# Optimization experiments

Measured on AMD Instinct MI355X. Metric: run time of the kernel, lower is better.

## Reference

```python
import jax, jax.numpy as jnp
import numpy as np

N_NODES = 100000
N_EDGES = 1000000
IN_DIM, HID_DIM, OUT_DIM = 64, 64, 128


def gcn_conv(x, W, b, src, dst, deg_inv_sqrt, n_nodes):
    # PyG GCNConv: x' = D^{-1/2} (A + I) D^{-1/2} (x W) + b
    xw = x @ W  # [N, out]
    norm = deg_inv_sqrt[src] * deg_inv_sqrt[dst]  # [E'] (edges incl. self-loops)
    msgs = xw[src] * norm[:, None]  # gather + scale, [E', out]
    out = jax.ops.segment_sum(msgs, dst, num_segments=n_nodes)
    return out + b


def setup_inputs() -> dict:
    key = jax.random.key(0)
    ks = jax.random.split(key, 8)
    x = jax.random.normal(ks[0], (N_NODES, IN_DIM), dtype=jnp.float32)
    edge_index = jax.random.randint(ks[1], (2, N_EDGES), 0, N_NODES, dtype=jnp.int64 if jax.config.read('jax_enable_x64') else jnp.int32)
    # Glorot-ish init for weights, zeros for biases (matches GCNConv defaults)
    def glorot(k, fan_in, fan_out):
        s = jnp.sqrt(6.0 / (fan_in + fan_out))
        return jax.random.uniform(k, (fan_in, fan_out), jnp.float32, -s, s)
    return {
        "x": x,
        "W1": glorot(ks[2], IN_DIM, HID_DIM), "b1": jnp.zeros((HID_DIM,), jnp.float32),
        "W2": glorot(ks[3], HID_DIM, HID_DIM), "b2": jnp.zeros((HID_DIM,), jnp.float32),
        "W3": glorot(ks[4], HID_DIM, OUT_DIM), "b3": jnp.zeros((OUT_DIM,), jnp.float32),
        "edge_index": edge_index,
    }


def reference(x, W1, b1, W2, b2, W3, b3, edge_index):
    n = x.shape[0]
    loop = jnp.arange(n, dtype=edge_index.dtype)
    src = jnp.concatenate([edge_index[0], loop])  # add self-loops
    dst = jnp.concatenate([edge_index[1], loop])
    deg = jax.ops.segment_sum(jnp.ones_like(dst, dtype=x.dtype), dst, num_segments=n)
    deg_inv_sqrt = jnp.where(deg > 0, jax.lax.rsqrt(deg), 0.0)
    # Dropout(p=0.5) is identity in eval mode
    h = jax.nn.relu(gcn_conv(x, W1, b1, src, dst, deg_inv_sqrt, n))
    h = jax.nn.relu(gcn_conv(h, W2, b2, src, dst, deg_inv_sqrt, n))
    return gcn_conv(h, W3, b3, src, dst, deg_inv_sqrt, n)
```

## Files before the change

### kernel.cpp

```cpp
#include <hip/hip_runtime.h>
#include <hip/hip_fp16.h>


#define NBMAX 512
#define EPB   4096


__global__ __launch_bounds__(256) void bin_hist(const int* __restrict__ dst,
                                                int* __restrict__ hist, int E, int NB) {
  __shared__ int cnt[NBMAX];
  for (int i = threadIdx.x; i < NB; i += 256) cnt[i] = 0;
  __syncthreads();
  int base = blockIdx.x * EPB;
  for (int it = 0; it < EPB; it += 256) {
    int e = base + it + threadIdx.x;
    if (e < E) atomicAdd(&cnt[dst[e] >> 8], 1);
  }
  __syncthreads();
  for (int i = threadIdx.x; i < NB; i += 256) hist[(size_t)blockIdx.x * NB + i] = cnt[i];
}

__global__ __launch_bounds__(256) void bucket_prefix(int* __restrict__ hist,
                                                     int* __restrict__ bucket_tot,
                                                     int nblk, int NB) {
  __shared__ int tmp[256];
  int b = blockIdx.x;
  int t = threadIdx.x;
  int v = (t < nblk) ? hist[(size_t)t * NB + b] : 0;
  tmp[t] = v;
  __syncthreads();
  for (int off = 1; off < 256; off <<= 1) {
    int a = (t >= off) ? tmp[t - off] : 0;
    __syncthreads();
    tmp[t] += a;
    __syncthreads();
  }
  if (t < nblk) hist[(size_t)t * NB + b] = tmp[t] - v;
  if (t == 255) bucket_tot[b] = tmp[255];
}

__global__ __launch_bounds__(512) void bucket_scan(const int* __restrict__ bucket_tot,
                                                   int* __restrict__ bucket_off, int NB, int E) {
  __shared__ int tmp[NBMAX];
  int t = threadIdx.x;
  int v = (t < NB) ? bucket_tot[t] : 0;
  tmp[t] = v;
  __syncthreads();
  for (int off = 1; off < 512; off <<= 1) {
    int a = (t >= off) ? tmp[t - off] : 0;
    __syncthreads();
    tmp[t] += a;
    __syncthreads();
  }
  if (t < NB) bucket_off[t] = tmp[t] - v;
  if (t == 0) bucket_off[NB] = E;
}

__global__ __launch_bounds__(256) void bin_scatter(const int* __restrict__ src,
                                                   const int* __restrict__ dst,
                                                   const int* __restrict__ chunk_excl,
                                                   const int* __restrict__ bucket_off,
                                                   int2* __restrict__ pairs, int E, int NB) {
  __shared__ int cur[NBMAX];
  for (int i = threadIdx.x; i < NB; i += 256)
    cur[i] = bucket_off[i] + chunk_excl[(size_t)blockIdx.x * NB + i];
  __syncthreads();
  int base = blockIdx.x * EPB;
  for (int it = 0; it < EPB; it += 256) {
    int e = base + it + threadIdx.x;
    if (e < E) {
      int d = dst[e];
      int pos = atomicAdd(&cur[d >> 8], 1);
      pairs[pos] = make_int2(src[e], d);
    }
  }
}

__global__ __launch_bounds__(256) void bucket_fill(const int2* __restrict__ pairs,
                                                   const int* __restrict__ bucket_off,
                                                   int* __restrict__ row_ptr,
                                                   int* __restrict__ csr_src,
                                                   float* __restrict__ dis, int n, int NB) {
  __shared__ int cnt[256];
  __shared__ int tmp[256];
  __shared__ int cur[256];
  int b = blockIdx.x;
  int t = threadIdx.x;
  int node_base = b << 8;
  int ebeg = bucket_off[b];
  int eend = bucket_off[b + 1];
  cnt[t] = 0;
  __syncthreads();
  for (int e = ebeg + t; e < eend; e += 256) {
    atomicAdd(&cnt[pairs[e].y - node_base], 1);
  }
  __syncthreads();
  int v = cnt[t];
  tmp[t] = v;
  __syncthreads();
  for (int off = 1; off < 256; off <<= 1) {
    int a = (t >= off) ? tmp[t - off] : 0;
    __syncthreads();
    tmp[t] += a;
    __syncthreads();
  }
  int excl = tmp[t] - v;
  int node = node_base + t;
  if (node < n) {
    row_ptr[node] = ebeg + excl;
    dis[node] = rsqrtf((float)v + 1.0f);
  }
  cur[t] = ebeg + excl;
  if (b == NB - 1 && t == 0) row_ptr[n] = eend;
  __syncthreads();
  for (int e = ebeg + t; e < eend; e += 256) {
    int2 p = pairs[e];
    int pos = atomicAdd(&cur[p.y - node_base], 1);
    csr_src[pos] = p.x;
  }
}


__device__ __forceinline__ unsigned int packh(float a, float b) {
  unsigned int lo = (unsigned int)__half_as_ushort(__float2half_rn(a));
  unsigned int hi = (unsigned int)__half_as_ushort(__float2half_rn(b));
  return lo | (hi << 16);
}

__device__ __forceinline__ void unpack_add(float& x0, float& x1, unsigned int u) {
  x0 += __half2float(__ushort_as_half((unsigned short)(u & 0xffffu)));
  x1 += __half2float(__ushort_as_half((unsigned short)(u >> 16)));
}


__global__ void prescale_h(const float* __restrict__ x, const float* __restrict__ dis,
                           unsigned short* __restrict__ xs, int n) {
  int i = blockIdx.x * blockDim.x + threadIdx.x;
  if (i >= n * 8) return;
  int row = i >> 3;
  float s = dis[row];
  const float4* p = (const float4*)(x + (size_t)i * 8);
  float4 f0 = p[0];
  float4 f1 = p[1];
  uint4 u;
  u.x = packh(f0.x * s, f0.y * s);
  u.y = packh(f0.z * s, f0.w * s);
  u.z = packh(f1.x * s, f1.y * s);
  u.w = packh(f1.z * s, f1.w * s);
  *(uint4*)(xs + (size_t)i * 8) = u;
}


__global__ __launch_bounds__(256) void gather64q(const int* __restrict__ row_ptr,
                                                 const int* __restrict__ csr_src,
                                                 const unsigned short* __restrict__ in,
                                                 const float* __restrict__ dis,
                                                 float* __restrict__ agg, int n) {
  int node = blockIdx.x * 16 + (threadIdx.x >> 4);
  int l15 = threadIdx.x & 15;
  int gbase = threadIdx.x & 48;
  if (node >= n) return;

  int beg = row_ptr[node];
  int end = row_ptr[node + 1];

  float a0 = 0.f, a1 = 0.f, a2 = 0.f, a3 = 0.f;

  {
    uint2 q = *(const uint2*)(in + (size_t)node * 64 + l15 * 4);
    unpack_add(a0, a1, q.x); unpack_add(a2, a3, q.y);
  }

  for (int kb = beg; kb < end; kb += 16) {
    int idx = (kb + l15 < end) ? csr_src[kb + l15] : 0;
    int cnt = end - kb; if (cnt > 16) cnt = 16;
    int rr = 0;
    for (; rr + 2 <= cnt; rr += 2) {
      int s0 = __shfl(idx, gbase + rr);
      int s1 = __shfl(idx, gbase + rr + 1);
      uint2 q0 = *(const uint2*)(in + (size_t)s0 * 64 + l15 * 4);
      uint2 q1 = *(const uint2*)(in + (size_t)s1 * 64 + l15 * 4);
      unpack_add(a0, a1, q0.x); unpack_add(a2, a3, q0.y);
      unpack_add(a0, a1, q1.x); unpack_add(a2, a3, q1.y);
    }
    if (rr < cnt) {
      int s0 = __shfl(idx, gbase + rr);
      uint2 q0 = *(const uint2*)(in + (size_t)s0 * 64 + l15 * 4);
      unpack_add(a0, a1, q0.x); unpack_add(a2, a3, q0.y);
    }
  }

  float sc = dis[node];
  *(float4*)&agg[(size_t)node * 64 + l15 * 4] =
      make_float4(a0 * sc, a1 * sc, a2 * sc, a3 * sc);
}


__device__ __forceinline__ void fma4(float4& a, float s, const float4 w) {
  a.x = fmaf(s, w.x, a.x);
  a.y = fmaf(s, w.y, a.y);
  a.z = fmaf(s, w.z, a.z);
  a.w = fmaf(s, w.w, a.w);
}

template <bool RELU, bool SCALE, bool OUTH>
__global__ __launch_bounds__(256, 4) void gemm64(const float* __restrict__ X,
                                                 const float* __restrict__ W,
                                                 const float* __restrict__ B,
                                                 const float* __restrict__ dis,
                                                 float* __restrict__ yF,
                                                 unsigned short* __restrict__ yH,
                                                 int n, int ldw) {
  __shared__ float Xs[64 * 68];
  __shared__ float Ws[64 * 64];
  int tid = threadIdx.x;
  int rb = blockIdx.x * 64;
  int cb = blockIdx.y * 64;

  for (int i = tid; i < 1024; i += 256) {
    int k = i >> 4, cq = (i & 15) << 2;
    *(float4*)&Ws[k * 64 + cq] = *(const float4*)&W[(size_t)k * ldw + cb + cq];
  }
  for (int i = tid; i < 1024; i += 256) {
    int r = i >> 4, kq = (i & 15) << 2;
    int gr = rb + r;
    float4 v = make_float4(0.f, 0.f, 0.f, 0.f);
    if (gr < n) v = *(const float4*)&X[(size_t)gr * 64 + kq];
    *(float4*)&Xs[r * 68 + kq] = v;
  }
  __syncthreads();

  int r0 = (tid >> 4) << 2;
  int c0 = (tid & 15) << 2;

  float4 a0 = make_float4(0.f, 0.f, 0.f, 0.f);
  float4 a1 = a0, a2 = a0, a3 = a0;

#pragma unroll 2
  for (int kc = 0; kc < 64; kc += 4) {
    float4 x0 = *(const float4*)&Xs[(r0 + 0) * 68 + kc];
    float4 x1 = *(const float4*)&Xs[(r0 + 1) * 68 + kc];
    float4 x2 = *(const float4*)&Xs[(r0 + 2) * 68 + kc];
    float4 x3 = *(const float4*)&Xs[(r0 + 3) * 68 + kc];
    float4 w0 = *(const float4*)&Ws[(kc + 0) * 64 + c0];
    float4 w1 = *(const float4*)&Ws[(kc + 1) * 64 + c0];
    float4 w2 = *(const float4*)&Ws[(kc + 2) * 64 + c0];
    float4 w3 = *(const float4*)&Ws[(kc + 3) * 64 + c0];
    fma4(a0, x0.x, w0); fma4(a0, x0.y, w1); fma4(a0, x0.z, w2); fma4(a0, x0.w, w3);
    fma4(a1, x1.x, w0); fma4(a1, x1.y, w1); fma4(a1, x1.z, w2); fma4(a1, x1.w, w3);
    fma4(a2, x2.x, w0); fma4(a2, x2.y, w1); fma4(a2, x2.z, w2); fma4(a2, x2.w, w3);
    fma4(a3, x3.x, w0); fma4(a3, x3.y, w1); fma4(a3, x3.z, w2); fma4(a3, x3.w, w3);
  }

  float4 bb = *(const float4*)&B[cb + c0];
  int gr0 = rb + r0;
#pragma unroll
  for (int ri = 0; ri < 4; ++ri) {
    int gr = gr0 + ri;
    if (gr >= n) break;
    float4 v = (ri == 0) ? a0 : (ri == 1) ? a1 : (ri == 2) ? a2 : a3;
    v.x += bb.x; v.y += bb.y; v.z += bb.z; v.w += bb.w;
    if (RELU) {
      v.x = fmaxf(v.x, 0.f); v.y = fmaxf(v.y, 0.f);
      v.z = fmaxf(v.z, 0.f); v.w = fmaxf(v.w, 0.f);
    }
    if (SCALE) {
      float s = dis[gr];
      v.x *= s; v.y *= s; v.z *= s; v.w *= s;
    }
    if (OUTH) {
      uint2 u;
      u.x = packh(v.x, v.y);
      u.y = packh(v.z, v.w);
      *(uint2*)(yH + (size_t)gr * ldw + cb + c0) = u;
    } else {
      *(float4*)&yF[(size_t)gr * ldw + cb + c0] = v;
    }
  }
}


extern "C" void kernel_launch(void* const* d_in, const int* in_sizes, int n_in,
                              void* d_out, int out_size, void* d_ws, size_t ws_size,
                              hipStream_t stream) {
  const float* x  = (const float*)d_in[0];
  const float* W1 = (const float*)d_in[1];
  const float* b1 = (const float*)d_in[2];
  const float* W2 = (const float*)d_in[3];
  const float* b2 = (const float*)d_in[4];
  const float* W3 = (const float*)d_in[5];
  const float* b3 = (const float*)d_in[6];
  const int*   ei = (const int*)d_in[7];

  const int n = in_sizes[0] / 64;
  const int E = in_sizes[7] / 2;
  const int* src = ei;
  const int* dst = ei + E;

  const int NB    = (n + 255) >> 8;
  const int nblkA = (E + EPB - 1) / EPB;

  float* dis = (float*)d_ws;
  unsigned short* bufIn = (unsigned short*)(dis + n);
  float* agg = (float*)(bufIn + (size_t)n * 64);
  int* row_ptr = (int*)(agg + (size_t)n * 64);
  int* csr_src = row_ptr + (n + 2);
  int2* pairs  = (int2*)(csr_src + E);
  int* hist       = (int*)(pairs + E);
  int* bucket_tot = hist + (size_t)nblkA * NB;
  int* bucket_off = bucket_tot + NB;
  float* out = (float*)d_out;

  dim3 blk(256);
  int gW = (n + 15) / 16;
  int gT = (n + 63) / 64;
  int gS = (n * 8 + 255) / 256;

  bin_hist<<<nblkA, blk, 0, stream>>>(dst, hist, E, NB);
  bucket_prefix<<<NB, blk, 0, stream>>>(hist, bucket_tot, nblkA, NB);
  bucket_scan<<<1, 512, 0, stream>>>(bucket_tot, bucket_off, NB, E);
  bin_scatter<<<nblkA, blk, 0, stream>>>(src, dst, hist, bucket_off, pairs, E, NB);
  bucket_fill<<<NB, blk, 0, stream>>>(pairs, bucket_off, row_ptr, csr_src, dis, n, NB);

  prescale_h<<<gS, blk, 0, stream>>>(x, dis, bufIn, n);

  gather64q<<<gW, blk, 0, stream>>>(row_ptr, csr_src, bufIn, dis, agg, n);
  gemm64<true, true, true><<<dim3(gT, 1), blk, 0, stream>>>(agg, W1, b1, dis, nullptr, bufIn, n, 64);

  gather64q<<<gW, blk, 0, stream>>>(row_ptr, csr_src, bufIn, dis, agg, n);
  gemm64<true, true, true><<<dim3(gT, 1), blk, 0, stream>>>(agg, W2, b2, dis, nullptr, bufIn, n, 64);

  gather64q<<<gW, blk, 0, stream>>>(row_ptr, csr_src, bufIn, dis, agg, n);
  gemm64<false, false, false><<<dim3(gT, 2), blk, 0, stream>>>(agg, W3, b3, dis, out, nullptr, n, 128);
}
```

Baseline: 273.5 us.

## Pack edge pairs, fuse prescale into bucket fill, unroll gather, drop GEMM X staging

Packs each (src, local dst) edge pair into one 32-bit int, which halves the scatter traffic. The src field is limited to 17 bits, so node ids must stay below 131072. The fp16 prescale of x is folded into bucket_fill, removing one kernel launch and a re-read of dis. The gather loop is fully unrolled in chunks of 16 neighbours, and the remainder is handled with masked loads. The GEMM now reads X rows directly from global memory instead of staging them in shared memory, which trades coalesced LDS staging for cached global reads.

```diff
diff --git a/kernel.cpp b/kernel.cpp
--- a/kernel.cpp
+++ b/kernel.cpp
@@ -60,7 +60,7 @@
                                                    const int* __restrict__ dst,
                                                    const int* __restrict__ chunk_excl,
                                                    const int* __restrict__ bucket_off,
-                                                   int2* __restrict__ pairs, int E, int NB) {
+                                                   int* __restrict__ pairs, int E, int NB) {
   __shared__ int cur[NBMAX];
   for (int i = threadIdx.x; i < NB; i += 256)
     cur[i] = bucket_off[i] + chunk_excl[(size_t)blockIdx.x * NB + i];
@@ -71,19 +71,34 @@
     if (e < E) {
       int d = dst[e];
       int pos = atomicAdd(&cur[d >> 8], 1);
-      pairs[pos] = make_int2(src[e], d);
-    }
-  }
-}
-
-__global__ __launch_bounds__(256) void bucket_fill(const int2* __restrict__ pairs,
+      pairs[pos] = src[e] | ((d & 255) << 17);
+    }
+  }
+}
+
+__device__ __forceinline__ unsigned int packh(float a, float b) {
+  unsigned int lo = (unsigned int)__half_as_ushort(__float2half_rn(a));
+  unsigned int hi = (unsigned int)__half_as_ushort(__float2half_rn(b));
+  return lo | (hi << 16);
+}
+
+__device__ __forceinline__ void unpack_add(float& x0, float& x1, unsigned int u) {
+  x0 += __half2float(__ushort_as_half((unsigned short)(u & 0xffffu)));
+  x1 += __half2float(__ushort_as_half((unsigned short)(u >> 16)));
+}
+
+__global__ __launch_bounds__(256) void bucket_fill(const int* __restrict__ pairs,
                                                    const int* __restrict__ bucket_off,
                                                    int* __restrict__ row_ptr,
                                                    int* __restrict__ csr_src,
-                                                   float* __restrict__ dis, int n, int NB) {
+                                                   float* __restrict__ dis,
+                                                   const float* __restrict__ x,
+                                                   unsigned short* __restrict__ xs,
+                                                   int n, int NB) {
   __shared__ int cnt[256];
   __shared__ int tmp[256];
   __shared__ int cur[256];
+  __shared__ float sdis[256];
   int b = blockIdx.x;
   int t = threadIdx.x;
   int node_base = b << 8;
@@ -92,7 +107,7 @@
   cnt[t] = 0;
   __syncthreads();
   for (int e = ebeg + t; e < eend; e += 256) {
-    atomicAdd(&cnt[pairs[e].y - node_base], 1);
+    atomicAdd(&cnt[(pairs[e] >> 17) & 255], 1);
   }
   __syncthreads();
   int v = cnt[t];
@@ -106,48 +121,35 @@
   }
   int excl = tmp[t] - v;
   int node = node_base + t;
+  float s = rsqrtf((float)v + 1.0f);
+  sdis[t] = s;
   if (node < n) {
     row_ptr[node] = ebeg + excl;
-    dis[node] = rsqrtf((float)v + 1.0f);
+    dis[node] = s;
   }
   cur[t] = ebeg + excl;
   if (b == NB - 1 && t == 0) row_ptr[n] = eend;
   __syncthreads();
   for (int e = ebeg + t; e < eend; e += 256) {
-    int2 p = pairs[e];
-    int pos = atomicAdd(&cur[p.y - node_base], 1);
-    csr_src[pos] = p.x;
-  }
-}
-
-
-__device__ __forceinline__ unsigned int packh(float a, float b) {
-  unsigned int lo = (unsigned int)__half_as_ushort(__float2half_rn(a));
-  unsigned int hi = (unsigned int)__half_as_ushort(__float2half_rn(b));
-  return lo | (hi << 16);
-}
-
-__device__ __forceinline__ void unpack_add(float& x0, float& x1, unsigned int u) {
-  x0 += __half2float(__ushort_as_half((unsigned short)(u & 0xffffu)));
-  x1 += __half2float(__ushort_as_half((unsigned short)(u >> 16)));
-}
-
-
-__global__ void prescale_h(const float* __restrict__ x, const float* __restrict__ dis,
-                           unsigned short* __restrict__ xs, int n) {
-  int i = blockIdx.x * blockDim.x + threadIdx.x;
-  if (i >= n * 8) return;
-  int row = i >> 3;
-  float s = dis[row];
-  const float4* p = (const float4*)(x + (size_t)i * 8);
-  float4 f0 = p[0];
-  float4 f1 = p[1];
-  uint4 u;
-  u.x = packh(f0.x * s, f0.y * s);
-  u.y = packh(f0.z * s, f0.w * s);
-  u.z = packh(f1.x * s, f1.y * s);
-  u.w = packh(f1.z * s, f1.w * s);
-  *(uint4*)(xs + (size_t)i * 8) = u;
+    int p = pairs[e];
+    int pos = atomicAdd(&cur[(p >> 17) & 255], 1);
+    csr_src[pos] = p & 0x1FFFF;
+  }
+  int rows = n - node_base;
+  if (rows > 256) rows = 256;
+  for (int i = t; i < rows * 8; i += 256) {
+    int r = i >> 3;
+    float sc = sdis[r];
+    const float4* p = (const float4*)(x + ((size_t)(node_base + r) * 64) + (i & 7) * 8);
+    float4 f0 = p[0];
+    float4 f1 = p[1];
+    uint4 u;
+    u.x = packh(f0.x * sc, f0.y * sc);
+    u.y = packh(f0.z * sc, f0.w * sc);
+    u.z = packh(f1.x * sc, f1.y * sc);
+    u.w = packh(f1.z * sc, f1.w * sc);
+    *(uint4*)(xs + (size_t)(node_base + r) * 64 + (i & 7) * 8) = u;
+  }
 }
 
 
@@ -171,11 +173,11 @@
     unpack_add(a0, a1, q.x); unpack_add(a2, a3, q.y);
   }
 
-  for (int kb = beg; kb < end; kb += 16) {
-    int idx = (kb + l15 < end) ? csr_src[kb + l15] : 0;
-    int cnt = end - kb; if (cnt > 16) cnt = 16;
-    int rr = 0;
-    for (; rr + 2 <= cnt; rr += 2) {
+  int k = beg;
+  for (; k + 16 <= end; k += 16) {
+    int idx = csr_src[k + l15];
+#pragma unroll
+    for (int rr = 0; rr < 16; rr += 2) {
       int s0 = __shfl(idx, gbase + rr);
       int s1 = __shfl(idx, gbase + rr + 1);
       uint2 q0 = *(const uint2*)(in + (size_t)s0 * 64 + l15 * 4);
@@ -183,10 +185,25 @@
       unpack_add(a0, a1, q0.x); unpack_add(a2, a3, q0.y);
       unpack_add(a0, a1, q1.x); unpack_add(a2, a3, q1.y);
     }
-    if (rr < cnt) {
+  }
+  int cnt = end - k;
+  if (cnt > 0) {
+    int ii = k + l15;
+    int last = end - 1;
+    ii = (ii < end) ? ii : last;
+    int idx = csr_src[ii];
+#pragma unroll
+    for (int rr = 0; rr < 16; rr += 2) {
       int s0 = __shfl(idx, gbase + rr);
+      int s1 = __shfl(idx, gbase + rr + 1);
       uint2 q0 = *(const uint2*)(in + (size_t)s0 * 64 + l15 * 4);
+      uint2 q1 = *(const uint2*)(in + (size_t)s1 * 64 + l15 * 4);
+      q0.x = (rr < cnt) ? q0.x : 0u;
+      q0.y = (rr < cnt) ? q0.y : 0u;
+      q1.x = (rr + 1 < cnt) ? q1.x : 0u;
+      q1.y = (rr + 1 < cnt) ? q1.y : 0u;
       unpack_add(a0, a1, q0.x); unpack_add(a2, a3, q0.y);
+      unpack_add(a0, a1, q1.x); unpack_add(a2, a3, q1.y);
     }
   }
 
@@ -211,7 +228,6 @@
                                                  float* __restrict__ yF,
                                                  unsigned short* __restrict__ yH,
                                                  int n, int ldw) {
-  __shared__ float Xs[64 * 68];
   __shared__ float Ws[64 * 64];
   int tid = threadIdx.x;
   int rb = blockIdx.x * 64;
@@ -221,27 +237,26 @@
     int k = i >> 4, cq = (i & 15) << 2;
     *(float4*)&Ws[k * 64 + cq] = *(const float4*)&W[(size_t)k * ldw + cb + cq];
   }
-  for (int i = tid; i < 1024; i += 256) {
-    int r = i >> 4, kq = (i & 15) << 2;
-    int gr = rb + r;
-    float4 v = make_float4(0.f, 0.f, 0.f, 0.f);
-    if (gr < n) v = *(const float4*)&X[(size_t)gr * 64 + kq];
-    *(float4*)&Xs[r * 68 + kq] = v;
-  }
   __syncthreads();
 
   int r0 = (tid >> 4) << 2;
   int c0 = (tid & 15) << 2;
+  int gr0 = rb + r0;
+
+  const float* xp0 = X + (size_t)min(gr0 + 0, n - 1) * 64;
+  const float* xp1 = X + (size_t)min(gr0 + 1, n - 1) * 64;
+  const float* xp2 = X + (size_t)min(gr0 + 2, n - 1) * 64;
+  const float* xp3 = X + (size_t)min(gr0 + 3, n - 1) * 64;
 
   float4 a0 = make_float4(0.f, 0.f, 0.f, 0.f);
   float4 a1 = a0, a2 = a0, a3 = a0;
 
 #pragma unroll 2
   for (int kc = 0; kc < 64; kc += 4) {
-    float4 x0 = *(const float4*)&Xs[(r0 + 0) * 68 + kc];
-    float4 x1 = *(const float4*)&Xs[(r0 + 1) * 68 + kc];
-    float4 x2 = *(const float4*)&Xs[(r0 + 2) * 68 + kc];
-    float4 x3 = *(const float4*)&Xs[(r0 + 3) * 68 + kc];
+    float4 x0 = *(const float4*)(xp0 + kc);
+    float4 x1 = *(const float4*)(xp1 + kc);
+    float4 x2 = *(const float4*)(xp2 + kc);
+    float4 x3 = *(const float4*)(xp3 + kc);
     float4 w0 = *(const float4*)&Ws[(kc + 0) * 64 + c0];
     float4 w1 = *(const float4*)&Ws[(kc + 1) * 64 + c0];
     float4 w2 = *(const float4*)&Ws[(kc + 2) * 64 + c0];
@@ -253,7 +268,6 @@
   }
 
   float4 bb = *(const float4*)&B[cb + c0];
-  int gr0 = rb + r0;
 #pragma unroll
   for (int ri = 0; ri < 4; ++ri) {
     int gr = gr0 + ri;
@@ -305,8 +319,8 @@
   float* agg = (float*)(bufIn + (size_t)n * 64);
   int* row_ptr = (int*)(agg + (size_t)n * 64);
   int* csr_src = row_ptr + (n + 2);
-  int2* pairs  = (int2*)(csr_src + E);
-  int* hist       = (int*)(pairs + E);
+  int* pairs   = csr_src + E;
+  int* hist       = pairs + E;
   int* bucket_tot = hist + (size_t)nblkA * NB;
   int* bucket_off = bucket_tot + NB;
   float* out = (float*)d_out;
@@ -314,15 +328,12 @@
   dim3 blk(256);
   int gW = (n + 15) / 16;
   int gT = (n + 63) / 64;
-  int gS = (n * 8 + 255) / 256;
 
   bin_hist<<<nblkA, blk, 0, stream>>>(dst, hist, E, NB);
   bucket_prefix<<<NB, blk, 0, stream>>>(hist, bucket_tot, nblkA, NB);
   bucket_scan<<<1, 512, 0, stream>>>(bucket_tot, bucket_off, NB, E);
   bin_scatter<<<nblkA, blk, 0, stream>>>(src, dst, hist, bucket_off, pairs, E, NB);
-  bucket_fill<<<NB, blk, 0, stream>>>(pairs, bucket_off, row_ptr, csr_src, dis, n, NB);
-
-  prescale_h<<<gS, blk, 0, stream>>>(x, dis, bufIn, n);
+  bucket_fill<<<NB, blk, 0, stream>>>(pairs, bucket_off, row_ptr, csr_src, dis, x, bufIn, n, NB);
 
   gather64q<<<gW, blk, 0, stream>>>(row_ptr, csr_src, bufIn, dis, agg, n);
   gemm64<true, true, true><<<dim3(gT, 1), blk, 0, stream>>>(agg, W1, b1, dis, nullptr, bufIn, n, 64);
```

After: 278.3 us. No clear change (+1.8%).
